# Kernel tuning notes

Measured on AMD Instinct MI355X. Metric: run time of the kernel, lower is better.

## Reference

```python
import jax, jax.numpy as jnp
import numpy as np

Q, N, FDIM, HDIM = 4096, 1024, 64, 128


def setup_inputs() -> dict:
    key = jax.random.key(0)
    ks = jax.random.split(key, 7)
    s = 0.05
    return {
        "query_points": jax.random.normal(ks[0], (Q, 3), dtype=jnp.float32),
        "node_features": jax.random.normal(ks[1], (N, FDIM), dtype=jnp.float32),
        "node_positions": jax.random.normal(ks[2], (N, 3), dtype=jnp.float32),
        # attention MLP: Linear(F+3 -> H), ReLU, Linear(H -> 1)
        "aW1": jax.random.normal(ks[3], (FDIM + 3, HDIM), dtype=jnp.float32) * s,
        "ab1": jnp.zeros((HDIM,), dtype=jnp.float32),
        "aW2": jax.random.normal(ks[4], (HDIM, 1), dtype=jnp.float32) * s,
        "ab2": jnp.zeros((1,), dtype=jnp.float32),
        # decoder MLP: Linear(F -> H), ReLU, Linear(H -> 3)
        "dW1": jax.random.normal(ks[5], (FDIM, HDIM), dtype=jnp.float32) * s,
        "db1": jnp.zeros((HDIM,), dtype=jnp.float32),
        "dW2": jax.random.normal(ks[6], (HDIM, 3), dtype=jnp.float32) * s,
        "db2": jnp.zeros((3,), dtype=jnp.float32),
    }


def reference(query_points, node_features, node_positions,
              aW1, ab1, aW2, ab2, dW1, db1, dW2, db2):
    F = node_features.shape[1]
    # pairwise offsets: [Q, N, 3]
    diff = query_points[:, None, :] - node_positions[None, :, :]
    # xy-plane distance -> inverse-distance weights: [Q, N, 1]
    dist = jnp.linalg.norm(diff[..., :2], axis=-1, keepdims=True)
    w = 1.0 / (dist + 1e-6)
    # attn MLP on concat([node_features, diff]); split W1 so the feature
    # part ([N,F]@[F,H]) is computed once instead of per query pair.
    h = jax.nn.relu(node_features @ aW1[:F] + diff @ aW1[F:] + ab1)  # [Q, N, H]
    score = h @ aW2 + ab2                                            # [Q, N, 1]
    attn = jax.nn.softmax(score * w, axis=1)                         # [Q, N, 1]
    agg = jnp.einsum('qn,nf->qf', attn[..., 0], node_features)       # [Q, F]
    return jax.nn.relu(agg @ dW1 + db1) @ dW2 + db2                  # [Q, 3]
```

## Files before the change

kernel.cpp:

```cpp
#include <hip/hip_runtime.h>
#include <math.h>

#define QN 4096
#define NN 1024
#define FD 64
#define HD 128

typedef float v2f __attribute__((ext_vector_type(2)));
typedef float v4f __attribute__((ext_vector_type(4)));

#define OFF_UT4   0
#define OFF_B     524288
#define OFF_VU    655360
#define OFF_VB    659456
#define OFF_L     660480
#define OFF_PM    4854784
#define OFF_PART  5116928
#define OFF_SPART 7214080

__global__ __launch_bounds__(256) void k0_prep(
    const float* __restrict__ qp, const float* __restrict__ nf,
    const float* __restrict__ npos, const float* __restrict__ aW1,
    const float* __restrict__ ab1, const float* __restrict__ aW2,
    float* __restrict__ B, float* __restrict__ UT4,
    float* __restrict__ vu, float* __restrict__ vb) {
  int bid = blockIdx.x, t = threadIdx.x;
  if (bid < 2048) {
    int idx = bid * 256 + t;
    int j = idx & 3, q = (idx >> 2) & 4095, h4 = idx >> 14;
    int h = h4 * 4 + j;
    float u = qp[q*3+0] * aW1[(FD+0)*HD + h]
            + qp[q*3+1] * aW1[(FD+1)*HD + h]
            + qp[q*3+2] * aW1[(FD+2)*HD + h];
    UT4[idx] = u;
  } else if (bid < 2560) {
    int i2 = (bid - 2048) * 256 + t;
    int n = i2 >> 7, h = i2 & 127;
    float s = ab1[h];
    #pragma unroll
    for (int f = 0; f < FD; ++f) s = fmaf(nf[n*FD+f], aW1[f*HD+h], s);
    s -= npos[n*3+0] * aW1[(FD+0)*HD + h]
       + npos[n*3+1] * aW1[(FD+1)*HD + h]
       + npos[n*3+2] * aW1[(FD+2)*HD + h];
    B[i2] = s;
    float pv = s * aW2[h];
    #pragma unroll
    for (int m = 1; m < 64; m <<= 1) pv += __shfl_xor(pv, m, 64);
    __shared__ float ps[4];
    if ((t & 63) == 0) ps[t >> 6] = pv;
    __syncthreads();
    if (t == 0)   vb[n] = ps[0] + ps[1];
    if (t == 128) vb[n] = ps[2] + ps[3];
  } else {
    int q = (bid - 2560) * 256 + t;
    float q0 = qp[q*3+0], q1 = qp[q*3+1], q2 = qp[q*3+2];
    float acc = 0.f;
    #pragma unroll
    for (int h = 0; h < HD; ++h) {
      float u = q0 * aW1[(FD+0)*HD + h]
              + q1 * aW1[(FD+1)*HD + h]
              + q2 * aW1[(FD+2)*HD + h];
      acc = fmaf(aW2[h], u, acc);
    }
    vu[q] = acc;
  }
}


#define LOADU(dst) { \
  _Pragma("unroll") for (int qq = 0; qq < 4; ++qq) { \
    dst[qq][0] = p0[qq*64]; \
    dst[qq][1] = p1[qq*64]; } \
  p0 += 8192; p1 += 8192; }

#define COMPUTE(u) { \
  _Pragma("unroll") for (int nn = 0; nn < 4; ++nn) { \
    v4f b0 = bsb[(nb + nn)*32]; \
    v4f b1 = bsb[(nb + nn)*32 + 1]; \
    v2f b01 = __builtin_shufflevector(b0, b0, 0, 1); \
    v2f b23 = __builtin_shufflevector(b0, b0, 2, 3); \
    v2f b45 = __builtin_shufflevector(b1, b1, 0, 1); \
    v2f b67 = __builtin_shufflevector(b1, b1, 2, 3); \
    _Pragma("unroll") for (int qq = 0; qq < 4; ++qq) { \
      v2f u01 = __builtin_shufflevector(u[qq][0], u[qq][0], 0, 1); \
      v2f u23 = __builtin_shufflevector(u[qq][0], u[qq][0], 2, 3); \
      v2f u45 = __builtin_shufflevector(u[qq][1], u[qq][1], 0, 1); \
      v2f u67 = __builtin_shufflevector(u[qq][1], u[qq][1], 2, 3); \
      v2f t0, t1, t2, t3; \
      asm("v_pk_add_f32 %0, %1, %2" : "=v"(t0) : "v"(u01), "v"(b01)); \
      asm("v_pk_add_f32 %0, %1, %2" : "=v"(t1) : "v"(u23), "v"(b23)); \
      asm("v_pk_add_f32 %0, %1, %2" : "=v"(t2) : "v"(u45), "v"(b45)); \
      asm("v_pk_add_f32 %0, %1, %2" : "=v"(t3) : "v"(u67), "v"(b67)); \
      float a = acc[qq][nn]; \
      a = fmaf(aw[0], __builtin_fabsf(t0.x), a); \
      a = fmaf(aw[1], __builtin_fabsf(t0.y), a); \
      a = fmaf(aw[2], __builtin_fabsf(t1.x), a); \
      a = fmaf(aw[3], __builtin_fabsf(t1.y), a); \
      a = fmaf(aw[4], __builtin_fabsf(t2.x), a); \
      a = fmaf(aw[5], __builtin_fabsf(t2.y), a); \
      a = fmaf(aw[6], __builtin_fabsf(t3.x), a); \
      a = fmaf(aw[7], __builtin_fabsf(t3.y), a); \
      acc[qq][nn] = a; } } \
  bsb += 2; aw += 8; }

__global__ __launch_bounds__(256) void k2_logits(
    const float* __restrict__ Bg, const float* __restrict__ UT4,
    const float* __restrict__ aW2, const float* __restrict__ ab2,
    const float* __restrict__ qp, const float* __restrict__ npos,
    const float* __restrict__ vu, const float* __restrict__ vb,
    float* __restrict__ L, float* __restrict__ pm) {
  __shared__ float Bs[16 * HD];
  __shared__ float red[4][4][64];
  const int q0 = blockIdx.x * 256, n0 = blockIdx.y * 16;
  const int t = threadIdx.x;
  {
    const float4* src = (const float4*)(Bg + n0 * HD);
    float4* dst = (float4*)Bs;
    #pragma unroll
    for (int r = 0; r < 2; ++r) dst[r*256 + t] = src[r*256 + t];
  }
  __syncthreads();
  const int lane = t & 63, w = t >> 6;
  const int nb = w * 4;

  float acc[4][4];
  #pragma unroll
  for (int qq = 0; qq < 4; ++qq)
    #pragma unroll
    for (int nn = 0; nn < 4; ++nn) acc[qq][nn] = 0.f;

  const v4f* p0 = (const v4f*)UT4 + q0 + lane;
  const v4f* p1 = p0 + 4096;
  const v4f* bsb = (const v4f*)Bs;
  const float* aw = aW2;

  v4f uA[4][2], uB[4][2];
  LOADU(uA);
  #pragma unroll 1
  for (int hc = 0; hc < 14; hc += 2) {
    LOADU(uB);
    COMPUTE(uA);
    LOADU(uA);
    COMPUTE(uB);
  }
  LOADU(uB);
  COMPUTE(uA);
  COMPUTE(uB);

  const float bias2 = ab2[0];
  float qx[4], qy[4], vuq[4], m4[4];
  #pragma unroll
  for (int qq = 0; qq < 4; ++qq) {
    int q = q0 + qq*64 + lane;
    qx[qq] = qp[q*3+0];
    qy[qq] = qp[q*3+1];
    vuq[qq] = vu[q];
    m4[qq] = -3.4e38f;
  }
  #pragma unroll
  for (int nn = 0; nn < 4; ++nn) {
    int n = n0 + nb + nn;
    float px = npos[n*3+0], py = npos[n*3+1];
    float vbn = vb[n];
    #pragma unroll
    for (int qq = 0; qq < 4; ++qq) {
      float dx = qx[qq] - px, dy = qy[qq] - py;
      float wgt = 1.f / (sqrtf(dx*dx + dy*dy) + 1e-6f);
      float score = fmaf(0.5f, vuq[qq] + vbn + acc[qq][nn], bias2);
      float lg = score * wgt;
      L[n * QN + q0 + qq*64 + lane] = lg;
      m4[qq] = fmaxf(m4[qq], lg);
    }
  }
  #pragma unroll
  for (int qq = 0; qq < 4; ++qq) red[w][qq][lane] = m4[qq];
  __syncthreads();
  {
    int qq = t >> 6, ll = t & 63;
    float mm = fmaxf(fmaxf(red[0][qq][ll], red[1][qq][ll]),
                     fmaxf(red[2][qq][ll], red[3][qq][ll]));
    pm[blockIdx.y * QN + q0 + qq*64 + ll] = mm;
  }
}

__global__ __launch_bounds__(256) void k4_agg(
    const float* __restrict__ L, const float* __restrict__ pm,
    const float* __restrict__ nf, float* __restrict__ part,
    float* __restrict__ spart) {
  __shared__ float red[4][32][65];
  __shared__ float sred[4][64];
  int b = blockIdx.x;
  int qt = b & 63, c = b >> 6;
  int t = threadIdx.x, lane = t & 63, w = t >> 6;
  int q = qt * 64 + lane;

  float m = -3.4e38f;
  #pragma unroll
  for (int c64 = 0; c64 < 64; ++c64) m = fmaxf(m, pm[c64 * QN + q]);

  float acc[64];
  #pragma unroll
  for (int f = 0; f < 64; ++f) acc[f] = 0.f;
  float s = 0.f;

  int nbase = c * 128 + w * 32;
  float cur = L[nbase * QN + q];
  for (int i = 0; i < 32; ++i) {
    int n = nbase + i;
    float nxt = (i < 31) ? L[(n + 1) * QN + q] : 0.f;
    float p = exp2f((cur - m) * 1.44269504088896f);
    s += p;
    const float4* nfr = (const float4*)(nf + n * FD);
    #pragma unroll
    for (int g = 0; g < 4; ++g) {
      float4 a0 = nfr[g*4+0], a1 = nfr[g*4+1], a2 = nfr[g*4+2], a3 = nfr[g*4+3];
      acc[g*16+ 0] = fmaf(p, a0.x, acc[g*16+ 0]);
      acc[g*16+ 1] = fmaf(p, a0.y, acc[g*16+ 1]);
      acc[g*16+ 2] = fmaf(p, a0.z, acc[g*16+ 2]);
      acc[g*16+ 3] = fmaf(p, a0.w, acc[g*16+ 3]);
      acc[g*16+ 4] = fmaf(p, a1.x, acc[g*16+ 4]);
      acc[g*16+ 5] = fmaf(p, a1.y, acc[g*16+ 5]);
      acc[g*16+ 6] = fmaf(p, a1.z, acc[g*16+ 6]);
      acc[g*16+ 7] = fmaf(p, a1.w, acc[g*16+ 7]);
      acc[g*16+ 8] = fmaf(p, a2.x, acc[g*16+ 8]);
      acc[g*16+ 9] = fmaf(p, a2.y, acc[g*16+ 9]);
      acc[g*16+10] = fmaf(p, a2.z, acc[g*16+10]);
      acc[g*16+11] = fmaf(p, a2.w, acc[g*16+11]);
      acc[g*16+12] = fmaf(p, a3.x, acc[g*16+12]);
      acc[g*16+13] = fmaf(p, a3.y, acc[g*16+13]);
      acc[g*16+14] = fmaf(p, a3.z, acc[g*16+14]);
      acc[g*16+15] = fmaf(p, a3.w, acc[g*16+15]);
    }
    cur = nxt;
  }

  sred[w][lane] = s;
  #pragma unroll
  for (int f = 0; f < 32; ++f) red[w][f][lane] = acc[f];
  __syncthreads();
  for (int idx = t; idx < 2048; idx += 256) {
    int qq = idx >> 5, fr = idx & 31;
    float sum = red[0][fr][qq] + red[1][fr][qq] + red[2][fr][qq] + red[3][fr][qq];
    part[(c * QN + qt*64 + qq) * 64 + fr] = sum;
  }
  __syncthreads();
  #pragma unroll
  for (int f = 0; f < 32; ++f) red[w][f][lane] = acc[32 + f];
  __syncthreads();
  for (int idx = t; idx < 2048; idx += 256) {
    int qq = idx >> 5, fr = idx & 31;
    float sum = red[0][fr][qq] + red[1][fr][qq] + red[2][fr][qq] + red[3][fr][qq];
    part[(c * QN + qt*64 + qq) * 64 + 32 + fr] = sum;
  }
  __syncthreads();
  if (t < 64) {
    spart[c * QN + qt*64 + t] = sred[0][t] + sred[1][t] + sred[2][t] + sred[3][t];
  }
}

__global__ __launch_bounds__(256) void k5_dec(
    const float* __restrict__ part, const float* __restrict__ spart,
    const float* __restrict__ dW1, const float* __restrict__ db1,
    const float* __restrict__ dW2, const float* __restrict__ db2,
    float* __restrict__ out) {
  __shared__ float agg[16][64];
  __shared__ float inv[16];
  __shared__ float h1s[16][128];
  int t = threadIdx.x;
  int qb = blockIdx.x * 16;
  if (t < 16) {
    float s = 0.f;
    #pragma unroll
    for (int c = 0; c < 8; ++c) s += spart[c*QN + qb + t];
    inv[t] = 1.f / s;
  }
  {
    int f = t & 63, qh = t >> 6;
    #pragma unroll
    for (int pass = 0; pass < 4; ++pass) {
      int qs = pass*4 + qh;
      float v = 0.f;
      #pragma unroll
      for (int c = 0; c < 8; ++c) v += part[(c*QN + qb + qs)*64 + f];
      agg[qs][f] = v;
    }
  }
  __syncthreads();
  {
    int h = t & 127, qg = t >> 7;
    #pragma unroll
    for (int k = 0; k < 8; ++k) {
      int qs = qg*8 + k;
      float a = 0.f;
      #pragma unroll
      for (int f = 0; f < 64; ++f) a = fmaf(agg[qs][f], dW1[f*HD + h], a);
      h1s[qs][h] = fmaxf(a * inv[qs] + db1[h], 0.f);
    }
  }
  __syncthreads();
  if (t < 48) {
    int qs = t / 3, o = t % 3;
    float a = db2[o];
    #pragma unroll
    for (int h = 0; h < HD; ++h) a = fmaf(h1s[qs][h], dW2[h*3 + o], a);
    out[(qb + qs)*3 + o] = a;
  }
}

extern "C" void kernel_launch(void* const* d_in, const int* in_sizes, int n_in,
                              void* d_out, int out_size, void* d_ws, size_t ws_size,
                              hipStream_t stream) {
  const float* qp   = (const float*)d_in[0];
  const float* nf   = (const float*)d_in[1];
  const float* npos = (const float*)d_in[2];
  const float* aW1  = (const float*)d_in[3];
  const float* ab1  = (const float*)d_in[4];
  const float* aW2  = (const float*)d_in[5];
  const float* ab2  = (const float*)d_in[6];
  const float* dW1  = (const float*)d_in[7];
  const float* db1  = (const float*)d_in[8];
  const float* dW2  = (const float*)d_in[9];
  const float* db2  = (const float*)d_in[10];

  float* ws    = (float*)d_ws;
  float* UT4   = ws + OFF_UT4;
  float* B     = ws + OFF_B;
  float* vu    = ws + OFF_VU;
  float* vb    = ws + OFF_VB;
  float* L     = ws + OFF_L;
  float* pm    = ws + OFF_PM;
  float* part  = ws + OFF_PART;
  float* spart = ws + OFF_SPART;

  hipLaunchKernelGGL(k0_prep, dim3(2576), dim3(256), 0, stream,
                     qp, nf, npos, aW1, ab1, aW2, B, UT4, vu, vb);
  hipLaunchKernelGGL(k2_logits, dim3(16, 64), dim3(256), 0, stream,
                     B, UT4, aW2, ab2, qp, npos, vu, vb, L, pm);
  hipLaunchKernelGGL(k4_agg, dim3(512), dim3(256), 0, stream, L, pm, nf, part, spart);
  hipLaunchKernelGGL(k5_dec, dim3(256), dim3(256), 0, stream,
                     part, spart, dW1, db1, dW2, db2, (float*)d_out);
}
```

Baseline: 99.79 us.

## Re-layout query projections per block and split aggregation features across lanes

The precomputed query projection buffer is now stored blocked per 256-query tile in pairs of hidden units, so each logits block reads one contiguous slab with v2f loads. The inline packed-add asm is replaced by plain vector adds, and the aW2 weights are hoisted into scalars. The aggregation kernel now splits the 64 features across two half-waves, using 32 accumulators per thread and twice as many blocks, which reduces register pressure and adds parallelism. In exchange each L element is loaded twice and the block-level reduction is restructured.

```diff
diff --git a/kernel.cpp b/kernel.cpp
--- a/kernel.cpp
+++ b/kernel.cpp
@@ -7,9 +7,8 @@
 #define HD 128
 
 typedef float v2f __attribute__((ext_vector_type(2)));
-typedef float v4f __attribute__((ext_vector_type(4)));
-
-#define OFF_UT4   0
+
+#define OFF_UB    0
 #define OFF_B     524288
 #define OFF_VU    655360
 #define OFF_VB    659456
@@ -22,17 +21,19 @@
     const float* __restrict__ qp, const float* __restrict__ nf,
     const float* __restrict__ npos, const float* __restrict__ aW1,
     const float* __restrict__ ab1, const float* __restrict__ aW2,
-    float* __restrict__ B, float* __restrict__ UT4,
+    float* __restrict__ B, float* __restrict__ UB,
     float* __restrict__ vu, float* __restrict__ vb) {
   int bid = blockIdx.x, t = threadIdx.x;
   if (bid < 2048) {
     int idx = bid * 256 + t;
-    int j = idx & 3, q = (idx >> 2) & 4095, h4 = idx >> 14;
-    int h = h4 * 4 + j;
+    int e = idx & 1, lane = (idx >> 1) & 63, qq = (idx >> 7) & 3;
+    int h2 = (idx >> 9) & 63, qblk = idx >> 15;
+    int q = qblk * 256 + qq * 64 + lane;
+    int h = h2 * 2 + e;
     float u = qp[q*3+0] * aW1[(FD+0)*HD + h]
             + qp[q*3+1] * aW1[(FD+1)*HD + h]
             + qp[q*3+2] * aW1[(FD+2)*HD + h];
-    UT4[idx] = u;
+    UB[idx] = u;
   } else if (bid < 2560) {
     int i2 = (bid - 2048) * 256 + t;
     int n = i2 >> 7, h = i2 & 127;
@@ -69,42 +70,37 @@
 
 #define LOADU(dst) { \
   _Pragma("unroll") for (int qq = 0; qq < 4; ++qq) { \
-    dst[qq][0] = p0[qq*64]; \
-    dst[qq][1] = p1[qq*64]; } \
-  p0 += 8192; p1 += 8192; }
+    dst[qq][0] = P0[qq*64]; \
+    dst[qq][1] = P0[qq*64 + 256]; \
+    dst[qq][2] = P1[qq*64]; \
+    dst[qq][3] = P1[qq*64 + 256]; } \
+  P0 += 1024; P1 += 1024; }
 
 #define COMPUTE(u) { \
+  float aw0 = aw[0], aw1 = aw[1], aw2 = aw[2], aw3 = aw[3]; \
+  float aw4 = aw[4], aw5 = aw[5], aw6 = aw[6], aw7 = aw[7]; \
   _Pragma("unroll") for (int nn = 0; nn < 4; ++nn) { \
-    v4f b0 = bsb[(nb + nn)*32]; \
-    v4f b1 = bsb[(nb + nn)*32 + 1]; \
-    v2f b01 = __builtin_shufflevector(b0, b0, 0, 1); \
-    v2f b23 = __builtin_shufflevector(b0, b0, 2, 3); \
-    v2f b45 = __builtin_shufflevector(b1, b1, 0, 1); \
-    v2f b67 = __builtin_shufflevector(b1, b1, 2, 3); \
+    v2f b0 = bsB[nn*64], b1 = bsB[nn*64 + 1]; \
+    v2f b2 = bsB[nn*64 + 2], b3 = bsB[nn*64 + 3]; \
     _Pragma("unroll") for (int qq = 0; qq < 4; ++qq) { \
-      v2f u01 = __builtin_shufflevector(u[qq][0], u[qq][0], 0, 1); \
-      v2f u23 = __builtin_shufflevector(u[qq][0], u[qq][0], 2, 3); \
-      v2f u45 = __builtin_shufflevector(u[qq][1], u[qq][1], 0, 1); \
-      v2f u67 = __builtin_shufflevector(u[qq][1], u[qq][1], 2, 3); \
-      v2f t0, t1, t2, t3; \
-      asm("v_pk_add_f32 %0, %1, %2" : "=v"(t0) : "v"(u01), "v"(b01)); \
-      asm("v_pk_add_f32 %0, %1, %2" : "=v"(t1) : "v"(u23), "v"(b23)); \
-      asm("v_pk_add_f32 %0, %1, %2" : "=v"(t2) : "v"(u45), "v"(b45)); \
-      asm("v_pk_add_f32 %0, %1, %2" : "=v"(t3) : "v"(u67), "v"(b67)); \
+      v2f t0 = u[qq][0] + b0; \
+      v2f t1 = u[qq][1] + b1; \
+      v2f t2 = u[qq][2] + b2; \
+      v2f t3 = u[qq][3] + b3; \
       float a = acc[qq][nn]; \
-      a = fmaf(aw[0], __builtin_fabsf(t0.x), a); \
-      a = fmaf(aw[1], __builtin_fabsf(t0.y), a); \
-      a = fmaf(aw[2], __builtin_fabsf(t1.x), a); \
-      a = fmaf(aw[3], __builtin_fabsf(t1.y), a); \
-      a = fmaf(aw[4], __builtin_fabsf(t2.x), a); \
-      a = fmaf(aw[5], __builtin_fabsf(t2.y), a); \
-      a = fmaf(aw[6], __builtin_fabsf(t3.x), a); \
-      a = fmaf(aw[7], __builtin_fabsf(t3.y), a); \
+      a = fmaf(aw0, __builtin_fabsf(t0.x), a); \
+      a = fmaf(aw1, __builtin_fabsf(t0.y), a); \
+      a = fmaf(aw2, __builtin_fabsf(t1.x), a); \
+      a = fmaf(aw3, __builtin_fabsf(t1.y), a); \
+      a = fmaf(aw4, __builtin_fabsf(t2.x), a); \
+      a = fmaf(aw5, __builtin_fabsf(t2.y), a); \
+      a = fmaf(aw6, __builtin_fabsf(t3.x), a); \
+      a = fmaf(aw7, __builtin_fabsf(t3.y), a); \
       acc[qq][nn] = a; } } \
-  bsb += 2; aw += 8; }
+  bsB += 4; aw += 8; }
 
 __global__ __launch_bounds__(256) void k2_logits(
-    const float* __restrict__ Bg, const float* __restrict__ UT4,
+    const float* __restrict__ Bg, const float* __restrict__ UB,
     const float* __restrict__ aW2, const float* __restrict__ ab2,
     const float* __restrict__ qp, const float* __restrict__ npos,
     const float* __restrict__ vu, const float* __restrict__ vb,
@@ -129,23 +125,23 @@
     #pragma unroll
     for (int nn = 0; nn < 4; ++nn) acc[qq][nn] = 0.f;
 
-  const v4f* p0 = (const v4f*)UT4 + q0 + lane;
-  const v4f* p1 = p0 + 4096;
-  const v4f* bsb = (const v4f*)Bs;
+  const v2f* P0 = (const v2f*)UB + (size_t)blockIdx.x * 16384 + lane;
+  const v2f* P1 = P0 + 512;
+  const v2f* bsB = (const v2f*)Bs + nb * 64;
   const float* aw = aW2;
 
-  v4f uA[4][2], uB[4][2];
+  v2f uA[4][4], uB4[4][4];
   LOADU(uA);
   #pragma unroll 1
   for (int hc = 0; hc < 14; hc += 2) {
-    LOADU(uB);
+    LOADU(uB4);
     COMPUTE(uA);
     LOADU(uA);
-    COMPUTE(uB);
-  }
-  LOADU(uB);
+    COMPUTE(uB4);
+  }
+  LOADU(uB4);
   COMPUTE(uA);
-  COMPUTE(uB);
+  COMPUTE(uB4);
 
   const float bias2 = ab2[0];
   float qx[4], qy[4], vuq[4], m4[4];
@@ -187,74 +183,57 @@
     const float* __restrict__ L, const float* __restrict__ pm,
     const float* __restrict__ nf, float* __restrict__ part,
     float* __restrict__ spart) {
-  __shared__ float red[4][32][65];
-  __shared__ float sred[4][64];
+  __shared__ float red[4][2][32][33];
+  __shared__ float sred[4][33];
   int b = blockIdx.x;
-  int qt = b & 63, c = b >> 6;
+  int qt = b & 127, c = b >> 7;
   int t = threadIdx.x, lane = t & 63, w = t >> 6;
-  int q = qt * 64 + lane;
+  int qi = lane & 31, fh = lane >> 5;
+  int q = qt * 32 + qi;
 
   float m = -3.4e38f;
   #pragma unroll
-  for (int c64 = 0; c64 < 64; ++c64) m = fmaxf(m, pm[c64 * QN + q]);
-
-  float acc[64];
-  #pragma unroll
-  for (int f = 0; f < 64; ++f) acc[f] = 0.f;
+  for (int k = 0; k < 64; ++k) m = fmaxf(m, pm[k * QN + q]);
+
+  float acc[32];
+  #pragma unroll
+  for (int f = 0; f < 32; ++f) acc[f] = 0.f;
   float s = 0.f;
 
   int nbase = c * 128 + w * 32;
-  float cur = L[nbase * QN + q];
+  const float* Lp = L + (size_t)nbase * QN + q;
+  float cur = *Lp;
   for (int i = 0; i < 32; ++i) {
-    int n = nbase + i;
-    float nxt = (i < 31) ? L[(n + 1) * QN + q] : 0.f;
+    float nxt = (i < 31) ? Lp[(size_t)(i + 1) * QN] : 0.f;
     float p = exp2f((cur - m) * 1.44269504088896f);
     s += p;
-    const float4* nfr = (const float4*)(nf + n * FD);
-    #pragma unroll
-    for (int g = 0; g < 4; ++g) {
-      float4 a0 = nfr[g*4+0], a1 = nfr[g*4+1], a2 = nfr[g*4+2], a3 = nfr[g*4+3];
-      acc[g*16+ 0] = fmaf(p, a0.x, acc[g*16+ 0]);
-      acc[g*16+ 1] = fmaf(p, a0.y, acc[g*16+ 1]);
-      acc[g*16+ 2] = fmaf(p, a0.z, acc[g*16+ 2]);
-      acc[g*16+ 3] = fmaf(p, a0.w, acc[g*16+ 3]);
-      acc[g*16+ 4] = fmaf(p, a1.x, acc[g*16+ 4]);
-      acc[g*16+ 5] = fmaf(p, a1.y, acc[g*16+ 5]);
-      acc[g*16+ 6] = fmaf(p, a1.z, acc[g*16+ 6]);
-      acc[g*16+ 7] = fmaf(p, a1.w, acc[g*16+ 7]);
-      acc[g*16+ 8] = fmaf(p, a2.x, acc[g*16+ 8]);
-      acc[g*16+ 9] = fmaf(p, a2.y, acc[g*16+ 9]);
-      acc[g*16+10] = fmaf(p, a2.z, acc[g*16+10]);
-      acc[g*16+11] = fmaf(p, a2.w, acc[g*16+11]);
-      acc[g*16+12] = fmaf(p, a3.x, acc[g*16+12]);
-      acc[g*16+13] = fmaf(p, a3.y, acc[g*16+13]);
-      acc[g*16+14] = fmaf(p, a3.z, acc[g*16+14]);
-      acc[g*16+15] = fmaf(p, a3.w, acc[g*16+15]);
+    const float4* nfr = (const float4*)(nf + (nbase + i) * FD + fh * 32);
+    #pragma unroll
+    for (int g = 0; g < 8; ++g) {
+      float4 a = nfr[g];
+      acc[g*4+0] = fmaf(p, a.x, acc[g*4+0]);
+      acc[g*4+1] = fmaf(p, a.y, acc[g*4+1]);
+      acc[g*4+2] = fmaf(p, a.z, acc[g*4+2]);
+      acc[g*4+3] = fmaf(p, a.w, acc[g*4+3]);
     }
     cur = nxt;
   }
 
-  sred[w][lane] = s;
-  #pragma unroll
-  for (int f = 0; f < 32; ++f) red[w][f][lane] = acc[f];
-  __syncthreads();
-  for (int idx = t; idx < 2048; idx += 256) {
-    int qq = idx >> 5, fr = idx & 31;
-    float sum = red[0][fr][qq] + red[1][fr][qq] + red[2][fr][qq] + red[3][fr][qq];
-    part[(c * QN + qt*64 + qq) * 64 + fr] = sum;
-  }
-  __syncthreads();
-  #pragma unroll
-  for (int f = 0; f < 32; ++f) red[w][f][lane] = acc[32 + f];
-  __syncthreads();
-  for (int idx = t; idx < 2048; idx += 256) {
-    int qq = idx >> 5, fr = idx & 31;
-    float sum = red[0][fr][qq] + red[1][fr][qq] + red[2][fr][qq] + red[3][fr][qq];
-    part[(c * QN + qt*64 + qq) * 64 + 32 + fr] = sum;
-  }
-  __syncthreads();
-  if (t < 64) {
-    spart[c * QN + qt*64 + t] = sred[0][t] + sred[1][t] + sred[2][t] + sred[3][t];
+  #pragma unroll
+  for (int fi = 0; fi < 32; ++fi) red[w][fh][fi][qi] = acc[fi];
+  if (fh == 0) sred[w][qi] = s;
+  __syncthreads();
+  #pragma unroll
+  for (int k = 0; k < 8; ++k) {
+    int idx = k * 256 + t;
+    int qq = idx >> 6, f = idx & 63;
+    int f1 = f >> 5, f0 = f & 31;
+    float sum = red[0][f1][f0][qq] + red[1][f1][f0][qq]
+              + red[2][f1][f0][qq] + red[3][f1][f0][qq];
+    part[((size_t)c * QN + qt*32 + qq) * 64 + f] = sum;
+  }
+  if (t < 32) {
+    spart[c * QN + qt*32 + t] = sred[0][t] + sred[1][t] + sred[2][t] + sred[3][t];
   }
 }
 
@@ -281,7 +260,7 @@
       int qs = pass*4 + qh;
       float v = 0.f;
       #pragma unroll
-      for (int c = 0; c < 8; ++c) v += part[(c*QN + qb + qs)*64 + f];
+      for (int c = 0; c < 8; ++c) v += part[((size_t)c*QN + qb + qs)*64 + f];
       agg[qs][f] = v;
     }
   }
@@ -323,7 +302,7 @@
   const float* db2  = (const float*)d_in[10];
 
   float* ws    = (float*)d_ws;
-  float* UT4   = ws + OFF_UT4;
+  float* UB    = ws + OFF_UB;
   float* B     = ws + OFF_B;
   float* vu    = ws + OFF_VU;
   float* vb    = ws + OFF_VB;
@@ -333,10 +312,10 @@
   float* spart = ws + OFF_SPART;
 
   hipLaunchKernelGGL(k0_prep, dim3(2576), dim3(256), 0, stream,
-                     qp, nf, npos, aW1, ab1, aW2, B, UT4, vu, vb);
+                     qp, nf, npos, aW1, ab1, aW2, B, UB, vu, vb);
   hipLaunchKernelGGL(k2_logits, dim3(16, 64), dim3(256), 0, stream,
-                     B, UT4, aW2, ab2, qp, npos, vu, vb, L, pm);
-  hipLaunchKernelGGL(k4_agg, dim3(512), dim3(256), 0, stream, L, pm, nf, part, spart);
+                     B, UB, aW2, ab2, qp, npos, vu, vb, L, pm);
+  hipLaunchKernelGGL(k4_agg, dim3(1024), dim3(256), 0, stream, L, pm, nf, part, spart);
   hipLaunchKernelGGL(k5_dec, dim3(256), dim3(256), 0, stream,
                      part, spart, dW1, db1, dW2, db2, (float*)d_out);
 }
```

New measurement: 104.3 us. 4.5% more time.

## Fuse aggregation and decoder via last-block atomic counter, halve per-thread feature slice

Applied to the files above, without the earlier changes.

Merges the softmax-weighted aggregation and the decoder MLP into one kernel. Each of the 8 node-chunk blocks for a query tile increments an atomic counter, and the last block to finish reduces the partials and runs the decoder. Aggregation threads now cover 32 queries by half of the features each (32 accumulators instead of 64), which doubles the grid to 1024 blocks and lowers register pressure. This removes one kernel launch but adds a memset of the counters, atomics and fences, and leaves the decoder tail serialized on the last block of each tile.

```diff
diff --git a/kernel.cpp b/kernel.cpp
--- a/kernel.cpp
+++ b/kernel.cpp
@@ -17,6 +17,7 @@
 #define OFF_PM    4854784
 #define OFF_PART  5116928
 #define OFF_SPART 7214080
+#define OFF_DONE  7246848
 
 __global__ __launch_bounds__(256) void k0_prep(
     const float* __restrict__ qp, const float* __restrict__ nf,
@@ -65,7 +66,6 @@
     vu[q] = acc;
   }
 }
-
 
 #define LOADU(dst) { \
   _Pragma("unroll") for (int qq = 0; qq < 4; ++qq) { \
@@ -134,18 +134,18 @@
   const v4f* bsb = (const v4f*)Bs;
   const float* aw = aW2;
 
-  v4f uA[4][2], uB[4][2];
+  v4f uA[4][2], uB4[4][2];
   LOADU(uA);
   #pragma unroll 1
   for (int hc = 0; hc < 14; hc += 2) {
-    LOADU(uB);
+    LOADU(uB4);
     COMPUTE(uA);
     LOADU(uA);
-    COMPUTE(uB);
-  }
-  LOADU(uB);
+    COMPUTE(uB4);
+  }
+  LOADU(uB4);
   COMPUTE(uA);
-  COMPUTE(uB);
+  COMPUTE(uB4);
 
   const float bias2 = ab2[0];
   float qx[4], qy[4], vuq[4], m4[4];
@@ -183,126 +183,118 @@
   }
 }
 
-__global__ __launch_bounds__(256) void k4_agg(
+__global__ __launch_bounds__(256) void kB_aggdec(
     const float* __restrict__ L, const float* __restrict__ pm,
-    const float* __restrict__ nf, float* __restrict__ part,
-    float* __restrict__ spart) {
-  __shared__ float red[4][32][65];
-  __shared__ float sred[4][64];
+    const float* __restrict__ nf,
+    const float* __restrict__ dW1, const float* __restrict__ db1,
+    const float* __restrict__ dW2, const float* __restrict__ db2,
+    float* __restrict__ part, float* __restrict__ spart,
+    unsigned* __restrict__ done, float* __restrict__ out) {
+  __shared__ union {
+    struct { float red[4][2][32][33]; float sred[4][33]; } p2;
+    struct { float agg[32][65]; float inv[32]; float h1s[32][128]; } p3;
+  } sm;
+  __shared__ int isLast;
   int b = blockIdx.x;
-  int qt = b & 63, c = b >> 6;
+  int qt = b & 127, c = b >> 7;
   int t = threadIdx.x, lane = t & 63, w = t >> 6;
-  int q = qt * 64 + lane;
+  int qi = lane & 31, fh = lane >> 5;
+  int q = qt * 32 + qi;
 
   float m = -3.4e38f;
   #pragma unroll
-  for (int c64 = 0; c64 < 64; ++c64) m = fmaxf(m, pm[c64 * QN + q]);
-
-  float acc[64];
-  #pragma unroll
-  for (int f = 0; f < 64; ++f) acc[f] = 0.f;
+  for (int k = 0; k < 64; ++k) m = fmaxf(m, pm[k * QN + q]);
+
+  float acc[32];
+  #pragma unroll
+  for (int f = 0; f < 32; ++f) acc[f] = 0.f;
   float s = 0.f;
 
   int nbase = c * 128 + w * 32;
-  float cur = L[nbase * QN + q];
+  const float* Lp = L + (size_t)nbase * QN + q;
+  float cur = *Lp;
   for (int i = 0; i < 32; ++i) {
-    int n = nbase + i;
-    float nxt = (i < 31) ? L[(n + 1) * QN + q] : 0.f;
+    float nxt = (i < 31) ? Lp[(size_t)(i + 1) * QN] : 0.f;
     float p = exp2f((cur - m) * 1.44269504088896f);
     s += p;
-    const float4* nfr = (const float4*)(nf + n * FD);
-    #pragma unroll
-    for (int g = 0; g < 4; ++g) {
-      float4 a0 = nfr[g*4+0], a1 = nfr[g*4+1], a2 = nfr[g*4+2], a3 = nfr[g*4+3];
-      acc[g*16+ 0] = fmaf(p, a0.x, acc[g*16+ 0]);
-      acc[g*16+ 1] = fmaf(p, a0.y, acc[g*16+ 1]);
-      acc[g*16+ 2] = fmaf(p, a0.z, acc[g*16+ 2]);
-      acc[g*16+ 3] = fmaf(p, a0.w, acc[g*16+ 3]);
-      acc[g*16+ 4] = fmaf(p, a1.x, acc[g*16+ 4]);
-      acc[g*16+ 5] = fmaf(p, a1.y, acc[g*16+ 5]);
-      acc[g*16+ 6] = fmaf(p, a1.z, acc[g*16+ 6]);
-      acc[g*16+ 7] = fmaf(p, a1.w, acc[g*16+ 7]);
-      acc[g*16+ 8] = fmaf(p, a2.x, acc[g*16+ 8]);
-      acc[g*16+ 9] = fmaf(p, a2.y, acc[g*16+ 9]);
-      acc[g*16+10] = fmaf(p, a2.z, acc[g*16+10]);
-      acc[g*16+11] = fmaf(p, a2.w, acc[g*16+11]);
-      acc[g*16+12] = fmaf(p, a3.x, acc[g*16+12]);
-      acc[g*16+13] = fmaf(p, a3.y, acc[g*16+13]);
-      acc[g*16+14] = fmaf(p, a3.z, acc[g*16+14]);
-      acc[g*16+15] = fmaf(p, a3.w, acc[g*16+15]);
+    const float4* nfr = (const float4*)(nf + (nbase + i) * FD + fh * 32);
+    #pragma unroll
+    for (int g = 0; g < 8; ++g) {
+      float4 a = nfr[g];
+      acc[g*4+0] = fmaf(p, a.x, acc[g*4+0]);
+      acc[g*4+1] = fmaf(p, a.y, acc[g*4+1]);
+      acc[g*4+2] = fmaf(p, a.z, acc[g*4+2]);
+      acc[g*4+3] = fmaf(p, a.w, acc[g*4+3]);
     }
     cur = nxt;
   }
 
-  sred[w][lane] = s;
-  #pragma unroll
-  for (int f = 0; f < 32; ++f) red[w][f][lane] = acc[f];
-  __syncthreads();
-  for (int idx = t; idx < 2048; idx += 256) {
-    int qq = idx >> 5, fr = idx & 31;
-    float sum = red[0][fr][qq] + red[1][fr][qq] + red[2][fr][qq] + red[3][fr][qq];
-    part[(c * QN + qt*64 + qq) * 64 + fr] = sum;
-  }
-  __syncthreads();
-  #pragma unroll
-  for (int f = 0; f < 32; ++f) red[w][f][lane] = acc[32 + f];
-  __syncthreads();
-  for (int idx = t; idx < 2048; idx += 256) {
-    int qq = idx >> 5, fr = idx & 31;
-    float sum = red[0][fr][qq] + red[1][fr][qq] + red[2][fr][qq] + red[3][fr][qq];
-    part[(c * QN + qt*64 + qq) * 64 + 32 + fr] = sum;
-  }
-  __syncthreads();
-  if (t < 64) {
-    spart[c * QN + qt*64 + t] = sred[0][t] + sred[1][t] + sred[2][t] + sred[3][t];
-  }
-}
-
-__global__ __launch_bounds__(256) void k5_dec(
-    const float* __restrict__ part, const float* __restrict__ spart,
-    const float* __restrict__ dW1, const float* __restrict__ db1,
-    const float* __restrict__ dW2, const float* __restrict__ db2,
-    float* __restrict__ out) {
-  __shared__ float agg[16][64];
-  __shared__ float inv[16];
-  __shared__ float h1s[16][128];
-  int t = threadIdx.x;
-  int qb = blockIdx.x * 16;
-  if (t < 16) {
-    float s = 0.f;
-    #pragma unroll
-    for (int c = 0; c < 8; ++c) s += spart[c*QN + qb + t];
-    inv[t] = 1.f / s;
-  }
+  #pragma unroll
+  for (int fi = 0; fi < 32; ++fi) sm.p2.red[w][fh][fi][qi] = acc[fi];
+  if (fh == 0) sm.p2.sred[w][qi] = s;
+  __syncthreads();
+  #pragma unroll
+  for (int k = 0; k < 8; ++k) {
+    int idx = k * 256 + t;
+    int qq = idx >> 6, f = idx & 63;
+    int f1 = f >> 5, f0 = f & 31;
+    float sum = sm.p2.red[0][f1][f0][qq] + sm.p2.red[1][f1][f0][qq]
+              + sm.p2.red[2][f1][f0][qq] + sm.p2.red[3][f1][f0][qq];
+    part[((size_t)c * QN + qt*32 + qq) * 64 + f] = sum;
+  }
+  if (t < 32) {
+    spart[c * QN + qt*32 + t] = sm.p2.sred[0][t] + sm.p2.sred[1][t]
+                              + sm.p2.sred[2][t] + sm.p2.sred[3][t];
+  }
+
+  __threadfence();
+  __syncthreads();
+  if (t == 0) {
+    unsigned old = __hip_atomic_fetch_add(&done[qt], 1u, __ATOMIC_ACQ_REL,
+                                          __HIP_MEMORY_SCOPE_AGENT);
+    isLast = (old == 7);
+  }
+  __syncthreads();
+  if (!isLast) return;
+  __threadfence();
+
+  const int qb = qt * 32;
   {
     int f = t & 63, qh = t >> 6;
     #pragma unroll
-    for (int pass = 0; pass < 4; ++pass) {
-      int qs = pass*4 + qh;
+    for (int k = 0; k < 8; ++k) {
+      int qs = qh * 8 + k;
       float v = 0.f;
       #pragma unroll
-      for (int c = 0; c < 8; ++c) v += part[(c*QN + qb + qs)*64 + f];
-      agg[qs][f] = v;
-    }
+      for (int cc = 0; cc < 8; ++cc)
+        v += part[((size_t)cc * QN + qb + qs) * 64 + f];
+      sm.p3.agg[qs][f] = v;
+    }
+  }
+  if (t < 32) {
+    float ssum = 0.f;
+    #pragma unroll
+    for (int cc = 0; cc < 8; ++cc) ssum += spart[cc * QN + qb + t];
+    sm.p3.inv[t] = 1.f / ssum;
   }
   __syncthreads();
   {
     int h = t & 127, qg = t >> 7;
     #pragma unroll
-    for (int k = 0; k < 8; ++k) {
-      int qs = qg*8 + k;
+    for (int k = 0; k < 16; ++k) {
+      int qs = qg * 16 + k;
       float a = 0.f;
       #pragma unroll
-      for (int f = 0; f < 64; ++f) a = fmaf(agg[qs][f], dW1[f*HD + h], a);
-      h1s[qs][h] = fmaxf(a * inv[qs] + db1[h], 0.f);
-    }
-  }
-  __syncthreads();
-  if (t < 48) {
+      for (int f = 0; f < 64; ++f) a = fmaf(sm.p3.agg[qs][f], dW1[f*HD + h], a);
+      sm.p3.h1s[qs][h] = fmaxf(a * sm.p3.inv[qs] + db1[h], 0.f);
+    }
+  }
+  __syncthreads();
+  if (t < 96) {
     int qs = t / 3, o = t % 3;
     float a = db2[o];
     #pragma unroll
-    for (int h = 0; h < HD; ++h) a = fmaf(h1s[qs][h], dW2[h*3 + o], a);
+    for (int h = 0; h < HD; ++h) a = fmaf(sm.p3.h1s[qs][h], dW2[h*3 + o], a);
     out[(qb + qs)*3 + o] = a;
   }
 }
@@ -331,12 +323,14 @@
   float* pm    = ws + OFF_PM;
   float* part  = ws + OFF_PART;
   float* spart = ws + OFF_SPART;
-
+  unsigned* done = (unsigned*)(ws + OFF_DONE);
+  float* out   = (float*)d_out;
+
+  hipMemsetAsync(done, 0, 128 * sizeof(unsigned), stream);
   hipLaunchKernelGGL(k0_prep, dim3(2576), dim3(256), 0, stream,
                      qp, nf, npos, aW1, ab1, aW2, B, UT4, vu, vb);
   hipLaunchKernelGGL(k2_logits, dim3(16, 64), dim3(256), 0, stream,
                      B, UT4, aW2, ab2, qp, npos, vu, vb, L, pm);
-  hipLaunchKernelGGL(k4_agg, dim3(512), dim3(256), 0, stream, L, pm, nf, part, spart);
-  hipLaunchKernelGGL(k5_dec, dim3(256), dim3(256), 0, stream,
-                     part, spart, dW1, db1, dW2, db2, (float*)d_out);
+  hipLaunchKernelGGL(kB_aggdec, dim3(1024), dim3(256), 0, stream,
+                     L, pm, nf, dW1, db1, dW2, db2, part, spart, done, out);
 }
```

New measurement: 218.4 us. 2.19x slower.
